# Optimization experiments

Hardware: AMD Instinct MI355X
Metric: run time of the kernel (lower is better)

The kernel has to match this reference:

```python
import jax, jax.numpy as jnp
import numpy as np

NC = 10      # num_classes
HID = 64     # hidden_layer_dim
CIN = 512    # input_channels
THRESH = 100 # _LABEL2MASK_THRESHOL


def setup_inputs() -> dict:
    key = jax.random.key(0)
    k = jax.random.split(key, 5)
    B, h, w = 4, 60, 80
    feature1 = jax.random.normal(k[0], (B, CIN, h, w), jnp.float32)
    feature2 = jax.random.normal(k[1], (B, CIN, h // 2, w // 2), jnp.float32)
    s_in = (2.0 / CIN) ** 0.5   # kaiming_normal_ fan_in for 1x1 conv
    s_h = (2.0 / HID) ** 0.5
    w1 = jax.random.normal(k[2], (HID, CIN), jnp.float32) * s_in
    b1 = jnp.zeros((HID,), jnp.float32)
    w2 = jax.random.normal(k[3], (HID, CIN), jnp.float32) * s_in
    b2 = jnp.zeros((HID,), jnp.float32)
    w3 = jax.random.normal(k[4], (NC + 1, HID), jnp.float32) * s_h
    b3 = jnp.zeros((NC + 1,), jnp.float32)
    return {"feature1": feature1, "feature2": feature2,
            "w1": w1, "b1": b1, "w2": w2, "b2": b2, "w3": w3, "b3": b3}


def _resize_bilinear(x, H, W):
    # torch nn.Upsample(mode='bilinear', align_corners=False) ~ jax.image.resize bilinear
    B, C = x.shape[0], x.shape[1]
    return jax.image.resize(x, (B, C, H, W), method="bilinear")


def _label2bbx(seg):
    # Vectorized replacement of the batch x class Python loop: fused masked
    # min/max reductions per (batch, class). Classes 1..NC-1, class 0 skipped,
    # exactly as in the original. Fixed output shape (B*(NC-1), 6); rows with
    # pixel count < THRESH are filled with -1 (jit-compatible padding).
    B, H, W = seg.shape
    cls = jnp.arange(1, NC)                                   # (NC-1,)
    mask = seg[:, None, :, :] == cls[None, :, None, None]     # (B, NC-1, H, W)
    xs = jnp.arange(W)
    ys = jnp.arange(H)
    count = mask.sum(axis=(-2, -1))                           # (B, NC-1)
    xmin = jnp.min(jnp.where(mask, xs[None, None, None, :], W), axis=(-2, -1))
    xmax = jnp.max(jnp.where(mask, xs[None, None, None, :], -1), axis=(-2, -1))
    ymin = jnp.min(jnp.where(mask, ys[None, None, :, None], H), axis=(-2, -1))
    ymax = jnp.max(jnp.where(mask, ys[None, None, :, None], -1), axis=(-2, -1))
    bids = jnp.broadcast_to(jnp.arange(B)[:, None], (B, NC - 1))
    clsb = jnp.broadcast_to(cls[None, :], (B, NC - 1))
    bbx = jnp.stack([bids, xmin, ymin, xmax, ymax, clsb], axis=-1)  # (B, NC-1, 6)
    valid = (count >= THRESH)[..., None]
    return jnp.where(valid, bbx, -1).reshape(B * (NC - 1), 6)


def reference(feature1, feature2, w1, b1, w2, b2, w3, b3):
    # 1x1 convs expressed as channel GEMMs
    f1 = jax.nn.relu(jnp.einsum('bchw,oc->bohw', feature1, w1) + b1[None, :, None, None])
    f2 = jax.nn.relu(jnp.einsum('bchw,oc->bohw', feature2, w2) + b2[None, :, None, None])
    h, w = feature1.shape[2], feature1.shape[3]
    f2 = _resize_bilinear(f2, h, w)           # Upsample x2
    inter = f1 + f2
    up = _resize_bilinear(inter, 8 * h, 8 * w)  # Upsample x8
    logits = jax.nn.relu(jnp.einsum('bchw,oc->bohw', up, w3) + b3[None, :, None, None])
    probability = jax.nn.softmax(logits, axis=1)   # Softmax2d = softmax over C
    segmentation = jnp.argmax(probability, axis=1)  # (B, H, W)
    bbx = _label2bbx(segmentation)
    return probability, segmentation, bbx
```

## Files before the change

kernel.cpp:

```cpp
#include <hip/hip_runtime.h>

#define DEVINL __device__ __forceinline__

namespace {

constexpr int NB   = 4;
constexpr int CINv = 512;
constexpr int HIDv = 64;
constexpr int NCl  = 11;
constexpr int h1v = 60, w1v = 80;
constexpr int h2v = 30, w2v = 40;
constexpr int Hf = 480, Wf = 640;
constexpr int PPB1 = h1v * w1v;
constexpr int PPB2 = h2v * w2v;
constexpr int NP1 = NB * PPB1;
constexpr int NP2 = NB * PPB2;
constexpr int PPBF = Hf * Wf;
constexpr int NPF = NB * PPBF;
constexpr int NSHARD = 16;

constexpr size_t WS_P1  = 0;
constexpr size_t WS_P2  = WS_P1 + 4ull * HIDv * NP1;
constexpr size_t WS_Z   = WS_P2 + 4ull * HIDv * NP2;
constexpr size_t WS_BBX = WS_Z + (size_t)NB * NCl * PPB1;

constexpr size_t OUT_SEG = (size_t)NB * NCl * PPBF;
constexpr size_t OUT_BBX = OUT_SEG + (size_t)NPF;

DEVINL int iclamp(int v, int lo, int hi) { return v < lo ? lo : (v > hi ? hi : v); }

template <int PPB, int NPIX>
DEVINL void gemm_wave(const float* __restrict__ F, const float* __restrict__ Wm,
                      float* __restrict__ P, int pxt, int og, int ks) {
  const int lane = threadIdx.x & 63;
  const int gp0 = pxt * 128 + lane * 2;
  const int gpc = (gp0 <= NPIX - 2) ? gp0 : (NPIX - 2);
  const int b = gpc / PPB, pb = gpc - b * PPB;
  const float* aB = F + ((size_t)b * CINv + ks * 128) * PPB + pb;
  const float* wB = Wm + (size_t)og * 8 * CINv + ks * 128;

  float acc[8][2];
#pragma unroll
  for (int j = 0; j < 8; ++j) { acc[j][0] = 0.f; acc[j][1] = 0.f; }

  float2 aP[2], aQ[2];
  float wP[2][8], wQ[2][8];

  aP[0] = *reinterpret_cast<const float2*>(aB);
  aP[1] = *reinterpret_cast<const float2*>(aB + (size_t)PPB);
#pragma unroll
  for (int j = 0; j < 8; ++j) {
    wP[0][j] = wB[j * CINv + 0];
    wP[1][j] = wB[j * CINv + 1];
  }

  for (int k = 0; k < 64; k += 2) {
    const int cN = 2 * (k + 1);
    aQ[0] = *reinterpret_cast<const float2*>(aB + (size_t)cN * PPB);
    aQ[1] = *reinterpret_cast<const float2*>(aB + (size_t)(cN + 1) * PPB);
#pragma unroll
    for (int j = 0; j < 8; ++j) {
      wQ[0][j] = wB[j * CINv + cN + 0];
      wQ[1][j] = wB[j * CINv + cN + 1];
    }
#pragma unroll
    for (int c = 0; c < 2; ++c) {
      const float2 av = aP[c];
#pragma unroll
      for (int j = 0; j < 8; ++j) {
        const float wv = wP[c][j];
        acc[j][0] = fmaf(av.x, wv, acc[j][0]);
        acc[j][1] = fmaf(av.y, wv, acc[j][1]);
      }
    }
    if (k + 2 < 64) {
      const int cM = 2 * (k + 2);
      aP[0] = *reinterpret_cast<const float2*>(aB + (size_t)cM * PPB);
      aP[1] = *reinterpret_cast<const float2*>(aB + (size_t)(cM + 1) * PPB);
#pragma unroll
      for (int j = 0; j < 8; ++j) {
        wP[0][j] = wB[j * CINv + cM + 0];
        wP[1][j] = wB[j * CINv + cM + 1];
      }
    }
#pragma unroll
    for (int c = 0; c < 2; ++c) {
      const float2 av = aQ[c];
#pragma unroll
      for (int j = 0; j < 8; ++j) {
        const float wv = wQ[c][j];
        acc[j][0] = fmaf(av.x, wv, acc[j][0]);
        acc[j][1] = fmaf(av.y, wv, acc[j][1]);
      }
    }
  }

  if (gp0 <= NPIX - 2) {
#pragma unroll
    for (int j = 0; j < 8; ++j) {
      float2 v;
      v.x = acc[j][0]; v.y = acc[j][1];
      *reinterpret_cast<float2*>(P + (size_t)(ks * 64 + og * 8 + j) * NPIX + gp0) = v;
    }
  }
}

__global__ __launch_bounds__(256) void k_gemm(const float* __restrict__ f1,
                                              const float* __restrict__ f2,
                                              const float* __restrict__ w1,
                                              const float* __restrict__ w2,
                                              float* __restrict__ ws) {
  const int bid = blockIdx.x;
  const int half = bid / 752;
  const int f = bid - half * 752;
  const int og = __builtin_amdgcn_readfirstlane(half * 4 + (threadIdx.x >> 6));

  if (f < 600) {
    gemm_wave<PPB1, NP1>(f1, w1, ws + WS_P1, f >> 2, og, f & 3);
  } else {
    const int g = f - 600;
    gemm_wave<PPB2, NP2>(f2, w2, ws + WS_P2, g >> 2, og, g & 3);
  }
}

__global__ __launch_bounds__(256) void k_combine_z(float* __restrict__ ws,
                                                   const float* __restrict__ b1,
                                                   const float* __restrict__ b2,
                                                   const float* __restrict__ w3,
                                                   const float* __restrict__ b3) {
  __shared__ float inter[64 * 32];
  __shared__ float w3s[NCl * HIDv];
  const int t = threadIdx.x;

  if (blockIdx.x == 0) {
    int* sh = (int*)(ws + WS_BBX);
    for (int i = t; i < NSHARD * 36 * 8; i += 256) {
      int f = i & 7;
      sh[i] = (f == 0 || f >= 5) ? 0
            : ((f == 1 || f == 3) ? 0x7fffffff : (int)0x80000000);
    }
  }
  for (int e = t; e < NCl * HIDv; e += 256) w3s[e] = w3[e];

  const int pxl = t & 31;
  const int qi = t >> 5;
  const int gp = blockIdx.x * 32 + pxl;
  const int b = gp / PPB1, pb = gp - b * PPB1;
  const int y = pb / w1v, x = pb - y * w1v;

  const float sx = x * 0.5f - 0.25f;
  const float x0f = floorf(sx);
  const float fx = sx - x0f;
  const int ix0 = iclamp((int)x0f, 0, w2v - 1);
  const int ix1 = iclamp((int)x0f + 1, 0, w2v - 1);
  const float sy = y * 0.5f - 0.25f;
  const float y0f = floorf(sy);
  const float fy = sy - y0f;
  const int iy0 = iclamp((int)y0f, 0, h2v - 1);
  const int iy1 = iclamp((int)y0f + 1, 0, h2v - 1);

  const float* p1 = ws + WS_P1;
  const float* p2 = ws + WS_P2;
  const int base2 = b * PPB2;
  const int i00 = base2 + iy0 * w2v + ix0;
  const int i01 = base2 + iy0 * w2v + ix1;
  const int i10 = base2 + iy1 * w2v + ix0;
  const int i11 = base2 + iy1 * w2v + ix1;

#pragma unroll
  for (int cc = 0; cc < 8; ++cc) {
    const int ch = qi * 8 + cc;
    float v = b1[ch];
#pragma unroll
    for (int s = 0; s < 4; ++s)
      v += p1[(size_t)(s * 64 + ch) * NP1 + gp];
    v = fmaxf(v, 0.f);
    float t00 = b2[ch], t01 = t00, t10 = t00, t11 = t00;
#pragma unroll
    for (int s = 0; s < 4; ++s) {
      const float* ps = p2 + (size_t)(s * 64 + ch) * NP2;
      t00 += ps[i00]; t01 += ps[i01]; t10 += ps[i10]; t11 += ps[i11];
    }
    const float v00 = fmaxf(t00, 0.f), v01 = fmaxf(t01, 0.f);
    const float v10 = fmaxf(t10, 0.f), v11 = fmaxf(t11, 0.f);
    const float top = v00 + fx * (v01 - v00);
    const float bot = v10 + fx * (v11 - v10);
    v += top + fy * (bot - top);
    inter[ch * 32 + pxl] = v;
  }
  __syncthreads();

  float* z = ws + WS_Z;
  {
    float a = b3[qi];
#pragma unroll
    for (int ch = 0; ch < 64; ++ch)
      a = fmaf(inter[ch * 32 + pxl], w3s[qi * HIDv + ch], a);
    z[((size_t)b * NCl + qi) * PPB1 + pb] = a;
  }
  if (qi < 3) {
    const int o = qi + 8;
    float a = b3[o];
#pragma unroll
    for (int ch = 0; ch < 64; ++ch)
      a = fmaf(inter[ch * 32 + pxl], w3s[o * HIDv + ch], a);
    z[((size_t)b * NCl + o) * PPB1 + pb] = a;
  }
}

__global__ __launch_bounds__(256) void k_up_softmax(const float* __restrict__ ws,
                                                    float* __restrict__ out,
                                                    int* __restrict__ shards) {
  constexpr int ZR = 3, ZC = 18, ZN = NCl * ZR * ZC;
  __shared__ float zt[ZN];
  __shared__ int sB[4][9][4];
  const int t = threadIdx.x;
  const int tile = blockIdx.x;
  const int tx = tile % 5;
  const int ty = (tile / 5) % 240;
  const int b  = tile / 1200;
  const int base_x = tx * 16 - 1;
  const int row0 = ty * 2;
  const int base_y = (int)floorf((row0 + 0.5f) * 0.125f - 0.5f);

  const float* zb = ws + WS_Z + (size_t)b * NCl * PPB1;
  for (int e = t; e < ZN; e += 256) {
    int ch = e / (ZR * ZC);
    int rc = e % (ZR * ZC);
    int row = rc / ZC, col = rc % ZC;
    int gr = iclamp(base_y + row, 0, h1v - 1);
    int gc = iclamp(base_x + col, 0, w1v - 1);
    zt[e] = zb[(size_t)ch * PPB1 + gr * w1v + gc];
  }
  __syncthreads();

  const int x  = t & 127;
  const int rr = t >> 7;
  const int X = tx * 128 + x;
  const int Y = row0 + rr;

  const float sy = (Y + 0.5f) * 0.125f - 0.5f;
  const int y0g = (int)floorf(sy);
  const float fy = sy - (float)y0g;
  const int lry = y0g - base_y;
  const int lcx = (2 * x + 9) >> 4;
  const float fx = (float)(2 * x - 7) * 0.0625f + 1.0f - (float)lcx;

  float lg[NCl];
  float m = -1.f;
  int bi = 0;
#pragma unroll
  for (int c = 0; c < NCl; ++c) {
    const int base = c * (ZR * ZC) + lry * ZC + lcx;
    float v00 = zt[base],      v01 = zt[base + 1];
    float v10 = zt[base + ZC], v11 = zt[base + ZC + 1];
    float l0 = v00 + fy * (v10 - v00);
    float l1 = v01 + fy * (v11 - v01);
    float v = fmaxf(l0 + fx * (l1 - l0), 0.f);
    lg[c] = v;
    if (v > m) { m = v; bi = c; }
  }

  float s = 0.f;
#pragma unroll
  for (int c = 0; c < NCl; ++c) {
    float e = __expf(lg[c] - m);
    lg[c] = e;
    s += e;
  }
  const float inv = __builtin_amdgcn_rcpf(s);

  const size_t r = (size_t)Y * Wf + X;
  float* prob = out + (size_t)b * NCl * PPBF;
#pragma unroll
  for (int c = 0; c < NCl; ++c)
    prob[(size_t)c * PPBF + r] = lg[c] * inv;
  out[OUT_SEG + (size_t)b * PPBF + r] = (float)bi;

  const int lane = t & 63;
  const int wv = t >> 6;
  int cw[9], xn[9], xx[9];
#pragma unroll
  for (int c = 1; c <= 9; ++c) {
    unsigned long long msk = __ballot(bi == c);
    cw[c - 1] = (int)__popcll(msk);
    xn[c - 1] = msk ? (int)__builtin_ctzll(msk) : 0;
    xx[c - 1] = msk ? 63 - (int)__builtin_clzll(msk) : 0;
  }
  if (lane == 0) {
#pragma unroll
    for (int c = 0; c < 9; ++c) {
      sB[wv][c][0] = cw[c];
      sB[wv][c][1] = X + xn[c];
      sB[wv][c][2] = X + xx[c];
      sB[wv][c][3] = Y;
    }
  }
  __syncthreads();
  if (t < 9) {
    int C = 0, mn = 0x7fffffff, mx = -1, yn = 0x7fffffff, yx = -1;
#pragma unroll
    for (int w2 = 0; w2 < 4; ++w2) {
      int cc = sB[w2][t][0];
      if (cc) {
        C += cc;
        mn = min(mn, sB[w2][t][1]); mx = max(mx, sB[w2][t][2]);
        yn = min(yn, sB[w2][t][3]); yx = max(yx, sB[w2][t][3]);
      }
    }
    if (C) {
      int* e = shards + (((tile & (NSHARD - 1)) * 36) + b * 9 + t) * 8;
      atomicAdd(e + 0, C);
      atomicMin(e + 1, mn);
      atomicMax(e + 2, mx);
      atomicMin(e + 3, yn);
      atomicMax(e + 4, yx);
    }
  }
}

__global__ void k_bbx_final(const int* __restrict__ sh, float* __restrict__ out) {
  const int t = threadIdx.x;
  if (t >= 36) return;
  int C = 0, xn = 0x7fffffff, xx = -1, yn = 0x7fffffff, yx = -1;
  for (int s = 0; s < NSHARD; ++s) {
    const int* e = sh + (s * 36 + t) * 8;
    int c = e[0];
    if (c) {
      C += c;
      xn = min(xn, e[1]); xx = max(xx, e[2]);
      yn = min(yn, e[3]); yx = max(yx, e[4]);
    }
  }
  float* o = out + OUT_BBX + t * 6;
  if (C >= 100) {
    o[0] = (float)(t / 9);
    o[1] = (float)xn;
    o[2] = (float)yn;
    o[3] = (float)xx;
    o[4] = (float)yx;
    o[5] = (float)(t % 9 + 1);
  } else {
    for (int i = 0; i < 6; ++i) o[i] = -1.f;
  }
}

}

extern "C" void kernel_launch(void* const* d_in, const int* in_sizes, int n_in,
                              void* d_out, int out_size, void* d_ws, size_t ws_size,
                              hipStream_t stream) {
  const float* f1 = (const float*)d_in[0];
  const float* f2 = (const float*)d_in[1];
  const float* w1 = (const float*)d_in[2];
  const float* b1 = (const float*)d_in[3];
  const float* w2 = (const float*)d_in[4];
  const float* b2 = (const float*)d_in[5];
  const float* w3 = (const float*)d_in[6];
  const float* b3 = (const float*)d_in[7];
  float* out = (float*)d_out;
  float* ws = (float*)d_ws;

  hipLaunchKernelGGL(k_gemm, dim3(1504), dim3(256), 0, stream, f1, f2, w1, w2, ws);
  hipLaunchKernelGGL(k_combine_z, dim3(600), dim3(256), 0, stream, ws, b1, b2, w3, b3);
  hipLaunchKernelGGL(k_up_softmax, dim3(4800), dim3(256), 0, stream, ws, out,
                     (int*)(ws + WS_BBX));
  hipLaunchKernelGGL(k_bbx_final, dim3(1), dim3(64), 0, stream,
                     (const int*)(ws + WS_BBX), out);
}
```

Baseline: 84.74 us.

## Stage GEMM activations through LDS with async global_load_lds double buffering

Rewrites the 1x1-conv GEMM so each block cooperatively copies 16-channel activation slices into double-buffered shared memory using async global-to-LDS loads. The four waves then share those activations instead of each wave reading them separately from global memory, and weights are loaded as float4. Block-wide barriers are added per stage, and the bbox shard count is raised from 16 to 64 to reduce atomic contention. The LDS layout, the stage indexing and the copy width of 16 need to line up exactly for the results to be correct.

Result: faster. 79.17 us (-6.6%).

```diff
diff --git a/kernel.cpp b/kernel.cpp
--- a/kernel.cpp
+++ b/kernel.cpp
@@ -17,7 +17,7 @@
 constexpr int NP2 = NB * PPB2;
 constexpr int PPBF = Hf * Wf;
 constexpr int NPF = NB * PPBF;
-constexpr int NSHARD = 16;
+constexpr int NSHARD = 64;
 
 constexpr size_t WS_P1  = 0;
 constexpr size_t WS_P2  = WS_P1 + 4ull * HIDv * NP1;
@@ -29,78 +29,84 @@
 
 DEVINL int iclamp(int v, int lo, int hi) { return v < lo ? lo : (v > hi ? hi : v); }
 
+DEVINL void async_copy16(const float* g_src, float* lds_dst) {
+  __builtin_amdgcn_global_load_lds(
+      (const __attribute__((address_space(1))) unsigned int*)g_src,
+      (__attribute__((address_space(3))) unsigned int*)lds_dst, 16, 0, 0);
+}
+
 template <int PPB, int NPIX>
-DEVINL void gemm_wave(const float* __restrict__ F, const float* __restrict__ Wm,
-                      float* __restrict__ P, int pxt, int og, int ks) {
-  const int lane = threadIdx.x & 63;
-  const int gp0 = pxt * 128 + lane * 2;
-  const int gpc = (gp0 <= NPIX - 2) ? gp0 : (NPIX - 2);
-  const int b = gpc / PPB, pb = gpc - b * PPB;
-  const float* aB = F + ((size_t)b * CINv + ks * 128) * PPB + pb;
-  const float* wB = Wm + (size_t)og * 8 * CINv + ks * 128;
+DEVINL void gemm_tile(const float* __restrict__ F, const float* __restrict__ Wm,
+                      float* __restrict__ P, int pxt, int ogg, int ks,
+                      float* __restrict__ Abuf ) {
+  const int t = threadIdx.x;
+  const int lane = t & 63;
+  const int w = __builtin_amdgcn_readfirstlane(t >> 6);
+
+  const int px_st = (t & 31) * 4;
+  const int cc0 = t >> 5;
+  const int gp_st = pxt * 128 + px_st;
+  const int gpc = (gp_st <= NPIX - 4) ? gp_st : (NPIX - 4);
+  const int b_st = gpc / PPB, pb_st = gpc - b_st * PPB;
+  const float* srcA0 = F + ((size_t)b_st * CINv + ks * 128 + cc0) * PPB + pb_st;
+  const float* srcA1 = srcA0 + (size_t)8 * PPB;
+  float* dstW = Abuf + w * 256;
+
+  const int p2 = (t & 63) * 2;
+  const float* wB = Wm + (size_t)(ogg * 32 + w * 8) * CINv + ks * 128;
 
   float acc[8][2];
 #pragma unroll
   for (int j = 0; j < 8; ++j) { acc[j][0] = 0.f; acc[j][1] = 0.f; }
 
-  float2 aP[2], aQ[2];
-  float wP[2][8], wQ[2][8];
-
-  aP[0] = *reinterpret_cast<const float2*>(aB);
-  aP[1] = *reinterpret_cast<const float2*>(aB + (size_t)PPB);
-#pragma unroll
-  for (int j = 0; j < 8; ++j) {
-    wP[0][j] = wB[j * CINv + 0];
-    wP[1][j] = wB[j * CINv + 1];
-  }
-
-  for (int k = 0; k < 64; k += 2) {
-    const int cN = 2 * (k + 1);
-    aQ[0] = *reinterpret_cast<const float2*>(aB + (size_t)cN * PPB);
-    aQ[1] = *reinterpret_cast<const float2*>(aB + (size_t)(cN + 1) * PPB);
-#pragma unroll
-    for (int j = 0; j < 8; ++j) {
-      wQ[0][j] = wB[j * CINv + cN + 0];
-      wQ[1][j] = wB[j * CINv + cN + 1];
-    }
-#pragma unroll
-    for (int c = 0; c < 2; ++c) {
-      const float2 av = aP[c];
-#pragma unroll
-      for (int j = 0; j < 8; ++j) {
-        const float wv = wP[c][j];
-        acc[j][0] = fmaf(av.x, wv, acc[j][0]);
-        acc[j][1] = fmaf(av.y, wv, acc[j][1]);
+#define STAGE(s, buf)                                                         \
+  {                                                                           \
+    const size_t koff = (size_t)(s) * 16 * PPB;                               \
+    async_copy16(srcA0 + koff, dstW + (buf) * 2048);                          \
+    async_copy16(srcA1 + koff, dstW + (buf) * 2048 + 1024);                   \
+  }
+
+  STAGE(0, 0)
+  __syncthreads();
+
+  int cur = 0;
+#pragma unroll 1
+  for (int s = 0; s < 8; ++s) {
+    if (s < 7) STAGE(s + 1, cur ^ 1)
+    const float* Ab = Abuf + cur * 2048;
+    const float* wS = wB + s * 16;
+#pragma unroll
+    for (int kq = 0; kq < 4; ++kq) {
+      float4 wq[8];
+#pragma unroll
+      for (int j = 0; j < 8; ++j)
+        wq[j] = *reinterpret_cast<const float4*>(wS + j * CINv + kq * 4);
+#pragma unroll
+      for (int kk = 0; kk < 4; ++kk) {
+        const float2 a =
+            *reinterpret_cast<const float2*>(Ab + (kq * 4 + kk) * 128 + p2);
+        const float* wqf = reinterpret_cast<const float*>(wq);
+#pragma unroll
+        for (int j = 0; j < 8; ++j) {
+          const float wv = wqf[j * 4 + kk];
+          acc[j][0] = fmaf(a.x, wv, acc[j][0]);
+          acc[j][1] = fmaf(a.y, wv, acc[j][1]);
+        }
       }
     }
-    if (k + 2 < 64) {
-      const int cM = 2 * (k + 2);
-      aP[0] = *reinterpret_cast<const float2*>(aB + (size_t)cM * PPB);
-      aP[1] = *reinterpret_cast<const float2*>(aB + (size_t)(cM + 1) * PPB);
-#pragma unroll
-      for (int j = 0; j < 8; ++j) {
-        wP[0][j] = wB[j * CINv + cM + 0];
-        wP[1][j] = wB[j * CINv + cM + 1];
-      }
-    }
-#pragma unroll
-    for (int c = 0; c < 2; ++c) {
-      const float2 av = aQ[c];
-#pragma unroll
-      for (int j = 0; j < 8; ++j) {
-        const float wv = wQ[c][j];
-        acc[j][0] = fmaf(av.x, wv, acc[j][0]);
-        acc[j][1] = fmaf(av.y, wv, acc[j][1]);
-      }
-    }
-  }
-
+    __syncthreads();
+    cur ^= 1;
+  }
+#undef STAGE
+
+  const int gp0 = pxt * 128 + p2;
   if (gp0 <= NPIX - 2) {
 #pragma unroll
     for (int j = 0; j < 8; ++j) {
       float2 v;
       v.x = acc[j][0]; v.y = acc[j][1];
-      *reinterpret_cast<float2*>(P + (size_t)(ks * 64 + og * 8 + j) * NPIX + gp0) = v;
+      *reinterpret_cast<float2*>(
+          P + (size_t)(ks * 64 + ogg * 32 + w * 8 + j) * NPIX + gp0) = v;
     }
   }
 }
@@ -110,16 +116,16 @@
                                               const float* __restrict__ w1,
                                               const float* __restrict__ w2,
                                               float* __restrict__ ws) {
+  __shared__ float Abuf[2 * 2048];
   const int bid = blockIdx.x;
-  const int half = bid / 752;
-  const int f = bid - half * 752;
-  const int og = __builtin_amdgcn_readfirstlane(half * 4 + (threadIdx.x >> 6));
+  const int ogg = bid / 752;
+  const int f = bid - ogg * 752;
 
   if (f < 600) {
-    gemm_wave<PPB1, NP1>(f1, w1, ws + WS_P1, f >> 2, og, f & 3);
+    gemm_tile<PPB1, NP1>(f1, w1, ws + WS_P1, f >> 2, ogg, f & 3, Abuf);
   } else {
     const int g = f - 600;
-    gemm_wave<PPB2, NP2>(f2, w2, ws + WS_P2, g >> 2, og, g & 3);
+    gemm_tile<PPB2, NP2>(f2, w2, ws + WS_P2, g >> 2, ogg, g & 3, Abuf);
   }
 }
 
```
